# Kernel tuning notes

Measured on AMD Instinct MI355X. Metric: run time of the kernel, lower is better.

## Reference

```python
import jax, jax.numpy as jnp
import numpy as np

VOCAB = 100000; D = 300; F_NUM = 768
M = 64; N = 16
SURF_L = 4; CTX_L = 50; DOC_L = 100; BODY_L = 200
HEADS = 5


def _conv_relu_avg(x, W, b):
    # x: [B, L, D] tokens-embedded; conv1d (valid) + relu + global avgpool -> [B, F]
    y = jax.lax.conv_general_dilated(x.transpose(0, 2, 1), W, (1,), 'VALID',
                                     dimension_numbers=('NCH', 'OIH', 'NCH'))
    return jax.nn.relu(y + b[None, :, None]).mean(axis=2)


def _mha(q, k, v, num_heads=HEADS):
    # split-head scaled dot-product attention (no learned projections), q:[Lq,D] k,v:[Lk,D]
    Lq, Dm = q.shape
    hd = Dm // num_heads
    qh = q.reshape(Lq, num_heads, hd).transpose(1, 0, 2)
    kh = k.reshape(k.shape[0], num_heads, hd).transpose(1, 0, 2)
    vh = v.reshape(v.shape[0], num_heads, hd).transpose(1, 0, 2)
    att = jax.nn.softmax(jnp.einsum('hqd,hkd->hqk', qh, kh) * (1.0 / np.sqrt(hd)), axis=-1)
    out = jnp.einsum('hqk,hkd->hqd', att, vh)
    return out.transpose(1, 0, 2).reshape(Lq, Dm)


def _cos(a, b, eps=1e-6):
    na = jnp.maximum(jnp.sqrt((a * a).sum(-1)), eps)
    nb = jnp.maximum(jnp.sqrt((b * b).sum(-1)), eps)
    return (a * b).sum(-1) / (na * nb)


def setup_inputs() -> dict:
    key = jax.random.key(0)
    ks = jax.random.split(key, 20)
    inp = {}
    inp['mention_entity'] = jnp.ones((M, N), dtype=jnp.int32)
    inp['m'] = M
    inp['n'] = N
    inp['mention_vec'] = jax.random.randint(ks[0], (M, SURF_L), 0, VOCAB)
    inp['context_vec'] = jax.random.randint(ks[1], (M, CTX_L), 0, VOCAB)
    inp['doc_vec'] = jax.random.randint(ks[2], (DOC_L,), 0, VOCAB)
    inp['title_vec'] = jax.random.normal(ks[3], (N, F_NUM), dtype=jnp.float32)
    inp['body_vec'] = jax.random.randint(ks[4], (N, BODY_L), 0, VOCAB)
    inp['sfeats'] = jnp.zeros((N, 1), dtype=jnp.float32)
    inp['m2c_prior'] = jax.random.uniform(ks[5], (N,), dtype=jnp.float32)
    inp['men2cands'] = jax.random.randint(ks[6], (M, N), 0, VOCAB)
    inp['contexts_ids'] = jax.random.randint(ks[7], (M, CTX_L), 0, VOCAB)
    inp['hand_features'] = jax.random.uniform(ks[8], (N, 1), dtype=jnp.float32)
    inp['bert_doc_vec'] = jax.random.normal(ks[9], (1, F_NUM), dtype=jnp.float32)
    # learned parameters
    inp['embed_table'] = jax.random.normal(ks[10], (VOCAB, D), dtype=jnp.float32) * 0.1
    inp['conv_ms_w'] = jax.random.normal(ks[11], (F_NUM, D, 2), dtype=jnp.float32) * 0.05
    inp['conv_ms_b'] = jnp.zeros((F_NUM,), dtype=jnp.float32)
    inp['conv_mc_w'] = jax.random.normal(ks[12], (F_NUM, D, 5), dtype=jnp.float32) * 0.05
    inp['conv_mc_b'] = jnp.zeros((F_NUM,), dtype=jnp.float32)
    inp['layer_local_w'] = jax.random.normal(ks[13], (7,), dtype=jnp.float32) * 0.3
    inp['layer_local_b'] = jnp.zeros((), dtype=jnp.float32)
    inp['att_w1'] = jax.random.normal(ks[14], (600, 300), dtype=jnp.float32) * 0.05
    inp['att_b1'] = jnp.zeros((300,), dtype=jnp.float32)
    inp['att_w2'] = jax.random.normal(ks[15], (300, 1), dtype=jnp.float32) * 0.05
    inp['att_b2'] = jnp.zeros((), dtype=jnp.float32)
    return inp


def reference(mention_entity, m, n, mention_vec, context_vec, doc_vec, title_vec,
              body_vec, sfeats, m2c_prior, men2cands, contexts_ids, hand_features,
              bert_doc_vec, embed_table, conv_ms_w, conv_ms_b, conv_mc_w, conv_mc_b,
              layer_local_w, layer_local_b, att_w1, att_b1, att_w2, att_b2):
    # per-mention conv features (vectorized over all mentions at once)
    ms = _conv_relu_avg(embed_table[mention_vec], conv_ms_w, conv_ms_b)   # [M,768]
    mc = _conv_relu_avg(embed_table[context_vec], conv_mc_w, conv_mc_b)   # [M,768]
    md = bert_doc_vec[0]                                                  # [768]
    doc_emb = embed_table[doc_vec]                                        # [100,300]
    body_emb = embed_table[body_vec]                                      # [N,200,300]

    # per-candidate cross attention doc<->body, max-pooled over query positions
    att_d_b = jax.vmap(lambda b: _mha(doc_emb, b, b).max(axis=0))(body_emb)          # [N,300]
    att_b_d = jax.vmap(lambda b: _mha(b, doc_emb, doc_emb).max(axis=0))(body_emb)    # [N,300]
    comb = jnp.concatenate([att_d_b, att_b_d], axis=-1)                              # [N,600]
    att_score = jax.nn.sigmoid(jax.nn.relu(comb @ att_w1 + att_b1) @ att_w2 + att_b2)[:, 0]  # [N]

    # LocalCtxAttRanker: candidate-vs-context attention score
    ctx_emb = embed_table[contexts_ids]                                   # [M,50,300]
    cand_emb = embed_table[men2cands]                                     # [M,N,300]
    tok = jnp.einsum('mnd,mtd->mnt', cand_emb, ctx_emb)                   # [M,N,50]
    p = jax.nn.softmax(tok.max(axis=1), axis=-1)                          # [M,50]
    ctxv = jnp.einsum('mt,mtd->md', p, ctx_emb)                           # [M,300]
    local_att = jnp.einsum('mnd,md->mn', cand_emb, ctxv)                  # [M,N]

    cos_st = _cos(ms[:, None, :], title_vec[None, :, :])                  # [M,N]
    cos_dt = _cos(md[None, :], title_vec)                                 # [N]
    cos_ct = _cos(mc[:, None, :], title_vec[None, :, :])                  # [M,N]

    Mm = ms.shape[0]
    bc = lambda v: jnp.broadcast_to(v[None, :], (Mm, v.shape[0]))
    # feature order matches torch.cat((hand_fea, prior, localAtt, attScore, C_score))
    feats = jnp.stack([bc(hand_features[:, 0]), bc(m2c_prior), local_att,
                       bc(att_score), cos_st, bc(cos_dt), cos_ct], axis=-1)  # [M,N,7]
    score = feats @ layer_local_w + layer_local_b                         # [M,N]

    # per-mention standardization (unbiased std, as torch.std), softmax and uniform renorm
    mu = score.mean(axis=1, keepdims=True)
    sd = score.std(axis=1, keepdims=True, ddof=1)
    z = (score - mu) / sd
    sm = jax.nn.softmax(z, axis=1)
    zmin = z.min(axis=1, keepdims=True)
    zmax = z.max(axis=1, keepdims=True)
    u = (z + 1.0 - zmin) / (zmax - zmin)
    u = u / u.sum(axis=1, keepdims=True)
    return (z, sm, u)
```

## Files before the change

kernel.cpp:

```cpp
#include <hip/hip_runtime.h>

#define MM 64
#define NN 16
#define DDIM 300
#define FNUM 768
#define SURF_LL 4
#define CTX_LL 50
#define DOC_LL 100
#define BODY_LL 200
#define NHEADS 5
#define HDIM 60

#define GM 2944
#define GK 1536
#define GN 768

typedef unsigned short u16;
typedef unsigned int u32;
typedef __attribute__((ext_vector_type(8))) short short8;
typedef __attribute__((ext_vector_type(4))) float f32x4;

#define OFF_MSG    0
#define OFF_CTX2G  76800
#define OFF_CANDG  1036800
#define OFF_MS     1344000
#define OFF_MC     1393152
#define OFF_PV0    1442304
#define OFF_PV1    1451904
#define OFF_ASC    1471104
#define OFF_LATT   1471120
#define OFF_ABF    1472144
#define OFF_WTMC   (OFF_ABF + GM*GK/2)
#define OFF_WTMS   (OFF_WTMC + GN*GK/2)
#define OFF_P      (OFF_WTMS + 600*768)

__device__ __forceinline__ u16 f2bf(float x) {
  union { float f; u32 u; } v; v.f = x;
  u32 r = v.u + 0x7FFFu + ((v.u >> 16) & 1u);
  return (u16)(r >> 16);
}

__global__ __launch_bounds__(256) void mega_prep_kernel(
    const float* __restrict__ embed,
    const int* __restrict__ mention_vec,
    const int* __restrict__ context_vec,
    const int* __restrict__ contexts_ids,
    const int* __restrict__ men2cands,
    const float* __restrict__ Wmc,
    const float* __restrict__ Wms,
    float* __restrict__ dst, float* __restrict__ mc,
    u32* __restrict__ Abf, u32* __restrict__ WTmc, float* __restrict__ WTms) {
  int bid = blockIdx.x;
  if (bid < 5250) {
    int e = bid * 256 + threadIdx.x;
    int row = e / DDIM;
    int col = e - row * DDIM;
    int tok;
    if (row < 256)       tok = mention_vec[row];
    else if (row < 3456) tok = contexts_ids[row - 256];
    else                 tok = men2cands[row - 3456];
    dst[e] = embed[(size_t)tok * DDIM + col];
  } else if (bid < 5442) {
    mc[(bid - 5250) * 256 + threadIdx.x] = 0.f;
  } else if (bid < 14274) {
    int idx = (bid - 5442) * 256 + threadIdx.x;
    int r = idx / (GK / 2);
    int kp = idx - r * (GK / 2);
    int k = kp * 2;
    int m = r / 46, t = r - m * 46;
    u32 out = 0;
#pragma unroll
    for (int j = 0; j < 2; j++) {
      int kj = k + j;
      u16 h = 0;
      if (kj < 1500) {
        int tap = kj / 300;
        int d = kj - tap * 300;
        int tok = context_vec[m * CTX_LL + t + tap];
        h = f2bf(embed[(size_t)tok * DDIM + d]);
      }
      out |= (u32)h << (16 * j);
    }
    Abf[idx] = out;
  } else if (bid < 16578) {
    int idx = (bid - 14274) * 256 + threadIdx.x;
    int n = idx / (GK / 2);
    int kp = idx - n * (GK / 2);
    int k = kp * 2;
    u32 out = 0;
#pragma unroll
    for (int j = 0; j < 2; j++) {
      int kj = k + j;
      u16 h = 0;
      if (kj < 1500) {
        int tap = kj / 300;
        int d = kj - tap * 300;
        h = f2bf(Wmc[(size_t)n * 1500 + d * 5 + tap]);
      }
      out |= (u32)h << (16 * j);
    }
    WTmc[idx] = out;
  } else {
    int idx = (bid - 16578) * 256 + threadIdx.x;
    int k = idx / FNUM;
    int f = idx - k * FNUM;
    WTms[idx] = Wms[(size_t)f * 600 + k];
  }
}

__global__ __launch_bounds__(256) void conv_gemm_kernel(
    const u16* __restrict__ A,
    const u16* __restrict__ B,
    const float* __restrict__ bias,
    float* __restrict__ mc) {
  int bn = blockIdx.x, bm = blockIdx.y;
  __shared__ u16 As[64][72];
  __shared__ u16 Bs[64][72];
  int tid = threadIdx.x;
  int w = tid >> 6, lane = tid & 63;
  int wr = w >> 1, wc = w & 1;
  int lg = lane >> 4, lm = lane & 15;
  f32x4 acc[2][2];
#pragma unroll
  for (int i = 0; i < 2; i++)
#pragma unroll
    for (int j = 0; j < 2; j++) acc[i][j] = (f32x4)0.f;
  int c0row = tid >> 3, ck = (tid & 7) * 8;
  const u16* Ag = A + (size_t)(bm * 64) * GK;
  const u16* Bg = B + (size_t)(bn * 64) * GK;
  for (int kt = 0; kt < GK / 64; kt++) {
    int k0 = kt * 64;
    uint4 av0 = *(const uint4*)(Ag + (size_t)c0row * GK + k0 + ck);
    uint4 av1 = *(const uint4*)(Ag + (size_t)(c0row + 32) * GK + k0 + ck);
    uint4 bv0 = *(const uint4*)(Bg + (size_t)c0row * GK + k0 + ck);
    uint4 bv1 = *(const uint4*)(Bg + (size_t)(c0row + 32) * GK + k0 + ck);
    __syncthreads();
    *(uint4*)&As[c0row][ck] = av0;
    *(uint4*)&As[c0row + 32][ck] = av1;
    *(uint4*)&Bs[c0row][ck] = bv0;
    *(uint4*)&Bs[c0row + 32][ck] = bv1;
    __syncthreads();
#pragma unroll
    for (int kk = 0; kk < 2; kk++) {
      short8 af0 = *(const short8*)&As[wr * 32 + lm][kk * 32 + lg * 8];
      short8 af1 = *(const short8*)&As[wr * 32 + 16 + lm][kk * 32 + lg * 8];
      short8 bf0 = *(const short8*)&Bs[wc * 32 + lm][kk * 32 + lg * 8];
      short8 bf1 = *(const short8*)&Bs[wc * 32 + 16 + lm][kk * 32 + lg * 8];
      acc[0][0] = __builtin_amdgcn_mfma_f32_16x16x32_bf16(af0, bf0, acc[0][0], 0, 0, 0);
      acc[0][1] = __builtin_amdgcn_mfma_f32_16x16x32_bf16(af0, bf1, acc[0][1], 0, 0, 0);
      acc[1][0] = __builtin_amdgcn_mfma_f32_16x16x32_bf16(af1, bf0, acc[1][0], 0, 0, 0);
      acc[1][1] = __builtin_amdgcn_mfma_f32_16x16x32_bf16(af1, bf1, acc[1][1], 0, 0, 0);
    }
  }
#pragma unroll
  for (int mf = 0; mf < 2; mf++)
#pragma unroll
    for (int nf = 0; nf < 2; nf++) {
      int col = bn * 64 + wc * 32 + nf * 16 + lm;
      float bb = bias[col];
      int base = bm * 64 + wr * 32 + mf * 16 + lg * 4;
      int mcur = base / 46;
      float s = 0.f;
#pragma unroll
      for (int r = 0; r < 4; r++) {
        float v = fmaxf(acc[mf][nf][r] + bb, 0.f) * (1.0f / 46.0f);
        int mm = (base + r) / 46;
        if (mm != mcur) { atomicAdd(&mc[mcur * FNUM + col], s); s = 0.f; mcur = mm; }
        s += v;
      }
      atomicAdd(&mc[mcur * FNUM + col], s);
    }
}

__device__ __forceinline__ void conv_ms_body(
    const float* __restrict__ msg, const float* __restrict__ WT,
    const float* __restrict__ B, float* __restrict__ ms, int b) {
  int m = b / 3, fi = b - m * 3;
  int f = fi * 256 + threadIdx.x;
  const float* x = msg + m * SURF_LL * DDIM;
  float a0 = 0.f, a1 = 0.f, a2 = 0.f;
  for (int d = 0; d < DDIM; d++) {
    float v0 = x[d], v1 = x[DDIM + d], v2 = x[2 * DDIM + d], v3 = x[3 * DDIM + d];
    float wA = WT[(size_t)(2 * d) * FNUM + f];
    float wB = WT[(size_t)(2 * d + 1) * FNUM + f];
    a0 += v0 * wA + v1 * wB;
    a1 += v1 * wA + v2 * wB;
    a2 += v2 * wA + v3 * wB;
  }
  float bb = B[f];
  float r = fmaxf(a0 + bb, 0.f) + fmaxf(a1 + bb, 0.f) + fmaxf(a2 + bb, 0.f);
  ms[m * FNUM + f] = r * (1.0f / 3.0f);
}

template <int DIR>
__device__ __forceinline__ void scores_body(
    const float* __restrict__ embed, const int* __restrict__ doc_vec,
    const int* __restrict__ body_vec, float* __restrict__ P, int b,
    float* __restrict__ smem) {
  constexpr int Lq = DIR ? 200 : 100;
  constexpr int Lk = DIR ? 100 : 200;
  constexpr int KPL = DIR ? 2 : 4;
  int qt = b / 80;
  int rem = b - qt * 80;
  int n = rem / 5, h = rem - n * 5;
  const int* qids = DIR ? body_vec + n * BODY_LL : doc_vec;
  const int* kids = DIR ? doc_vec : body_vec + n * BODY_LL;
  float* Ks = smem;
  float* Qs = smem + Lk * 62;
  for (int idx = threadIdx.x; idx < Lk * 15; idx += 256) {
    int r = idx / 15, c = idx - r * 15;
    float4 v = *(const float4*)(embed + (size_t)kids[r] * DDIM + h * HDIM + c * 4);
    float* dp = Ks + r * 62 + c * 4;
    dp[0] = v.x; dp[1] = v.y; dp[2] = v.z; dp[3] = v.w;
  }
  for (int idx = threadIdx.x; idx < 32 * 15; idx += 256) {
    int r = idx / 15, c = idx - r * 15;
    int q = qt * 32 + r; if (q >= Lq) q = Lq - 1;
    float4 v = *(const float4*)(embed + (size_t)qids[q] * DDIM + h * HDIM + c * 4);
    float* dp = Qs + r * 64 + c * 4;
    dp[0] = v.x; dp[1] = v.y; dp[2] = v.z; dp[3] = v.w;
  }
  __syncthreads();
  int w = threadIdx.x >> 6, lane = threadIdx.x & 63;
  int kcl[KPL];
#pragma unroll
  for (int j = 0; j < KPL; j++) {
    int kk = lane + 64 * j; kcl[j] = (kk < Lk) ? kk : (Lk - 1);
  }
  float acc[8][KPL];
#pragma unroll
  for (int i = 0; i < 8; i++)
#pragma unroll
    for (int j = 0; j < KPL; j++) acc[i][j] = 0.f;
  for (int d = 0; d < HDIM; d += 4) {
    float2 kva[KPL], kvb[KPL];
#pragma unroll
    for (int j = 0; j < KPL; j++) {
      kva[j] = *(const float2*)&Ks[kcl[j] * 62 + d];
      kvb[j] = *(const float2*)&Ks[kcl[j] * 62 + d + 2];
    }
#pragma unroll
    for (int i = 0; i < 8; i++) {
      float4 qv = *(const float4*)&Qs[(w * 8 + i) * 64 + d];
#pragma unroll
      for (int j = 0; j < KPL; j++)
        acc[i][j] += qv.x * kva[j].x + qv.y * kva[j].y +
                     qv.z * kvb[j].x + qv.w * kvb[j].y;
    }
  }
  const float scale = 0.12909944487358056f;
#pragma unroll
  for (int i = 0; i < 8; i++) {
    int q = qt * 32 + w * 8 + i;
    float mx = -1e30f;
#pragma unroll
    for (int j = 0; j < KPL; j++)
      if (lane + 64 * j < Lk) mx = fmaxf(mx, acc[i][j]);
#pragma unroll
    for (int o = 32; o >= 1; o >>= 1) mx = fmaxf(mx, __shfl_xor(mx, o));
    float mxs = mx * scale;
    float p[KPL];
    float s = 0.f;
#pragma unroll
    for (int j = 0; j < KPL; j++) {
      p[j] = (lane + 64 * j < Lk) ? __expf(acc[i][j] * scale - mxs) : 0.f;
      s += p[j];
    }
#pragma unroll
    for (int o = 32; o >= 1; o >>= 1) s += __shfl_xor(s, o);
    float inv = 1.0f / s;
    if (q < Lq) {
      float* rowp = P + (size_t)((n * 2 + DIR) * NHEADS + h) * 20000 + q * Lk;
#pragma unroll
      for (int j = 0; j < KPL; j++) {
        int kk = lane + 64 * j;
        if (kk < Lk) rowp[kk] = p[j] * inv;
      }
    }
  }
}

__device__ __forceinline__ void tokctxv_body(
    const float* __restrict__ candg, const float* __restrict__ ctx2g,
    float* __restrict__ local_att, int m, float* __restrict__ smem) {
  float* cand  = smem;
  float* ctx   = smem + 4800;
  float* tokb  = smem + 9600;
  float* tkmx  = smem + 9872;
  float* pp    = smem + 9936;
  float* sctxv = smem + 10000;
  int tid = threadIdx.x;
  for (int i = tid; i < NN * DDIM; i += 256)
    cand[i] = candg[(size_t)m * NN * DDIM + i];
  int nI = tid >> 4, tt = tid & 15;
  for (int tile = 0; tile < 4; tile++) {
    int cbase = tile * 16;
    __syncthreads();
    for (int i = tid; i < 16 * DDIM; i += 256) {
      int rr = i / DDIM, cc = i - rr * DDIM;
      int t = cbase + rr;
      ctx[rr * DDIM + cc] = (t < CTX_LL) ? ctx2g[(size_t)(m * CTX_LL + t) * DDIM + cc] : 0.f;
    }
    __syncthreads();
    const float4* ca = (const float4*)(cand + nI * DDIM);
    const float4* cb = (const float4*)(ctx + tt * DDIM);
    float dsum = 0.f;
#pragma unroll
    for (int c = 0; c < 75; c++) {
      float4 a = ca[c], b = cb[c];
      dsum += a.x * b.x + a.y * b.y + a.z * b.z + a.w * b.w;
    }
    tokb[nI * 17 + tt] = dsum;
    __syncthreads();
    if (tid < 16) {
      float mx = -1e30f;
      for (int nn = 0; nn < NN; nn++) mx = fmaxf(mx, tokb[nn * 17 + tid]);
      int t = cbase + tid;
      if (t < CTX_LL) tkmx[t] = mx;
    }
  }
  __syncthreads();
  if (tid < 64) {
    float v = (tid < CTX_LL) ? tkmx[tid] : -1e30f;
    float mx = v;
#pragma unroll
    for (int o = 32; o >= 1; o >>= 1) mx = fmaxf(mx, __shfl_xor(mx, o));
    float e = (tid < CTX_LL) ? expf(v - mx) : 0.f;
    float s = e;
#pragma unroll
    for (int o = 32; o >= 1; o >>= 1) s += __shfl_xor(s, o);
    pp[tid] = e / s;
  }
  __syncthreads();
  for (int d = tid; d < DDIM; d += 256) {
    float acc = 0.f;
    for (int t = 0; t < CTX_LL; t++)
      acc += pp[t] * ctx2g[(size_t)(m * CTX_LL + t) * DDIM + d];
    sctxv[d] = acc;
  }
  __syncthreads();
  int j = tid & 15;
  float dd = 0.f;
  for (int i = j; i < DDIM; i += 16) dd += cand[nI * DDIM + i] * sctxv[i];
#pragma unroll
  for (int o = 8; o >= 1; o >>= 1) dd += __shfl_xor(dd, o);
  if (j == 0) local_att[m * NN + nI] = dd;
}

__global__ __launch_bounds__(256) void mega_mid_kernel(
    const float* __restrict__ embed,
    const int* __restrict__ doc_vec,
    const int* __restrict__ body_vec,
    const float* __restrict__ msg,
    const float* __restrict__ WTms,
    const float* __restrict__ Bms,
    const float* __restrict__ candg,
    const float* __restrict__ ctx2g,
    float* __restrict__ ms,
    float* __restrict__ P,
    float* __restrict__ local_att) {
  __shared__ float smem[14448];
  int bid = blockIdx.x;
  if (bid < 192) {
    conv_ms_body(msg, WTms, Bms, ms, bid);
  } else if (bid < 512) {
    scores_body<0>(embed, doc_vec, body_vec, P, bid - 192, smem);
  } else if (bid < 1072) {
    scores_body<1>(embed, doc_vec, body_vec, P, bid - 512, smem);
  } else {
    tokctxv_body(candg, ctx2g, local_att, bid - 1072, smem);
  }
}

__global__ __launch_bounds__(256) void attn_pv_kernel(
    const float* __restrict__ embed,
    const int* __restrict__ doc_vec,
    const int* __restrict__ body_vec,
    const float* __restrict__ P,
    float* __restrict__ pv0,
    float* __restrict__ pv1) {
  int bid = blockIdx.x;
  int dir, pt, n, h;
  if (bid < 160) { dir = 0; h = bid % 5; n = (bid / 5) % 16; pt = bid / 80; }
  else { int b = bid - 160; dir = 1; h = b % 5; n = (b / 5) % 16; pt = b / 80; }
  int Lq = dir ? 200 : 100;
  int Lk = dir ? 100 : 200;
  int Lk4 = Lk >> 2;
  int K4STR = dir ? 27 : 51;
  const int* kids = dir ? doc_vec : body_vec + n * BODY_LL;
  __shared__ float4 Kt4[60 * 51];
  __shared__ float red[4][64];
  float* Ktf = (float*)Kt4;
  int RS = K4STR * 4;
  for (int idx = threadIdx.x; idx < Lk * 15; idx += 256) {
    int r = idx / 15, c = idx - r * 15;
    float4 v = *(const float4*)(embed + (size_t)kids[r] * DDIM + h * HDIM + c * 4);
    Ktf[(c * 4 + 0) * RS + r] = v.x;
    Ktf[(c * 4 + 1) * RS + r] = v.y;
    Ktf[(c * 4 + 2) * RS + r] = v.z;
    Ktf[(c * 4 + 3) * RS + r] = v.w;
  }
  __syncthreads();
  int lane = threadIdx.x & 63;
  int w = __builtin_amdgcn_readfirstlane(threadIdx.x >> 6);
  int dl = (lane < HDIM) ? lane : (HDIM - 1);
  const float4* Krow = Kt4 + dl * K4STR;
  const float* Pb = P + (size_t)((n * 2 + dir) * NHEADS + h) * 20000;
  float omax = -1e30f;
#pragma unroll
  for (int p = 0; p < 4; p++) {
    int q0 = pt * 64 + p * 16 + w * 4;
    int qa0 = min(q0, Lq - 1), qa1 = min(q0 + 1, Lq - 1);
    int qa2 = min(q0 + 2, Lq - 1), qa3 = min(q0 + 3, Lq - 1);
    const float4* P0 = (const float4*)(Pb + (size_t)qa0 * Lk);
    const float4* P1 = (const float4*)(Pb + (size_t)qa1 * Lk);
    const float4* P2 = (const float4*)(Pb + (size_t)qa2 * Lk);
    const float4* P3 = (const float4*)(Pb + (size_t)qa3 * Lk);
    float o0 = 0.f, o1 = 0.f, o2 = 0.f, o3 = 0.f;
    for (int k4 = 0; k4 < Lk4; k4++) {
      float4 pp0 = P0[k4], pp1 = P1[k4], pp2 = P2[k4], pp3 = P3[k4];
      float4 kk = Krow[k4];
      o0 += pp0.x * kk.x + pp0.y * kk.y + pp0.z * kk.z + pp0.w * kk.w;
      o1 += pp1.x * kk.x + pp1.y * kk.y + pp1.z * kk.z + pp1.w * kk.w;
      o2 += pp2.x * kk.x + pp2.y * kk.y + pp2.z * kk.z + pp2.w * kk.w;
      o3 += pp3.x * kk.x + pp3.y * kk.y + pp3.z * kk.z + pp3.w * kk.w;
    }
    if (q0 < Lq)     omax = fmaxf(omax, o0);
    if (q0 + 1 < Lq) omax = fmaxf(omax, o1);
    if (q0 + 2 < Lq) omax = fmaxf(omax, o2);
    if (q0 + 3 < Lq) omax = fmaxf(omax, o3);
  }
  red[threadIdx.x >> 6][lane] = omax;
  __syncthreads();
  if (threadIdx.x < 64 && lane < HDIM) {
    float m4 = fmaxf(fmaxf(red[0][lane], red[1][lane]),
                     fmaxf(red[2][lane], red[3][lane]));
    float* dst = dir ? pv1 + (size_t)((n * NHEADS + h) * 4 + pt) * HDIM
                     : pv0 + (size_t)((n * NHEADS + h) * 2 + pt) * HDIM;
    dst[lane] = m4;
  }
}

__global__ __launch_bounds__(256) void mlp_kernel(
    const float* __restrict__ pv0, const float* __restrict__ pv1,
    const float* __restrict__ w1, const float* __restrict__ b1,
    const float* __restrict__ w2, const float* __restrict__ b2,
    float* __restrict__ att_score) {
  int n = blockIdx.x, tid = threadIdx.x;
  __shared__ float comb[600];
  for (int idx = tid; idx < 300; idx += 256) {
    int h = idx / 60, d = idx - h * 60;
    float mx = -1e30f;
#pragma unroll
    for (int pt = 0; pt < 2; pt++)
      mx = fmaxf(mx, pv0[(size_t)((n * NHEADS + h) * 2 + pt) * HDIM + d]);
    comb[idx] = mx;
    mx = -1e30f;
#pragma unroll
    for (int pt = 0; pt < 4; pt++)
      mx = fmaxf(mx, pv1[(size_t)((n * NHEADS + h) * 4 + pt) * HDIM + d]);
    comb[300 + idx] = mx;
  }
  __syncthreads();
  float partial = 0.f;
  for (int j = tid; j < 300; j += 256) {
    float hh = b1[j];
    for (int k = 0; k < 600; k++) hh += comb[k] * w1[k * 300 + j];
    partial += fmaxf(hh, 0.f) * w2[j];
  }
  __shared__ float redd[256];
  redd[tid] = partial;
  __syncthreads();
  for (int s = 128; s > 0; s >>= 1) {
    if (tid < s) redd[tid] += redd[tid + s];
    __syncthreads();
  }
  if (tid == 0) att_score[n] = 1.0f / (1.0f + expf(-(redd[0] + b2[0])));
}

__global__ __launch_bounds__(256) void final_kernel(
    const float* __restrict__ ms,
    const float* __restrict__ mc,
    const float* __restrict__ title,
    const float* __restrict__ bert,
    const float* __restrict__ att_score,
    const float* __restrict__ m2c_prior,
    const float* __restrict__ hand,
    const float* __restrict__ local_att,
    const float* __restrict__ w7,
    const float* __restrict__ b7,
    float* __restrict__ out) {
  int m = blockIdx.x, tid = threadIdx.x;
  __shared__ float sms[FNUM], smc[FNUM], smd[FNUM];
  __shared__ float snorm[3], sscore[16], wred[3][4];
  for (int i = tid; i < FNUM; i += 256) {
    sms[i] = ms[m * FNUM + i];
    smc[i] = mc[m * FNUM + i];
    smd[i] = bert[i];
  }
  __syncthreads();
  float p1 = 0.f, p2 = 0.f, p3 = 0.f;
  for (int i = tid; i < FNUM; i += 256) {
    float a = sms[i], b = smc[i], c = smd[i];
    p1 += a * a; p2 += b * b; p3 += c * c;
  }
#pragma unroll
  for (int o = 32; o >= 1; o >>= 1) {
    p1 += __shfl_xor(p1, o); p2 += __shfl_xor(p2, o); p3 += __shfl_xor(p3, o);
  }
  int wid = tid >> 6, lane = tid & 63;
  if (lane == 0) { wred[0][wid] = p1; wred[1][wid] = p2; wred[2][wid] = p3; }
  __syncthreads();
  if (tid == 0) {
    snorm[0] = fmaxf(sqrtf(wred[0][0] + wred[0][1] + wred[0][2] + wred[0][3]), 1e-6f);
    snorm[1] = fmaxf(sqrtf(wred[1][0] + wred[1][1] + wred[1][2] + wred[1][3]), 1e-6f);
    snorm[2] = fmaxf(sqrtf(wred[2][0] + wred[2][1] + wred[2][2] + wred[2][3]), 1e-6f);
  }
  __syncthreads();
  int nI = tid >> 4, j = tid & 15;
  float d1 = 0.f, d2 = 0.f, d3 = 0.f, d4 = 0.f;
  for (int i = j; i < FNUM; i += 16) {
    float t = title[nI * FNUM + i];
    d1 += sms[i] * t; d2 += smc[i] * t; d3 += smd[i] * t; d4 += t * t;
  }
#pragma unroll
  for (int o = 8; o >= 1; o >>= 1) {
    d1 += __shfl_xor(d1, o); d2 += __shfl_xor(d2, o);
    d3 += __shfl_xor(d3, o); d4 += __shfl_xor(d4, o);
  }
  if (j == 0) {
    float nt = fmaxf(sqrtf(d4), 1e-6f);
    float cos_st = d1 / (snorm[0] * nt);
    float cos_ct = d2 / (snorm[1] * nt);
    float cos_dt = d3 / (snorm[2] * nt);
    float score = hand[nI] * w7[0] + m2c_prior[nI] * w7[1] +
                  local_att[m * NN + nI] * w7[2] + att_score[nI] * w7[3] +
                  cos_st * w7[4] + cos_dt * w7[5] + cos_ct * w7[6] + b7[0];
    sscore[nI] = score;
  }
  __syncthreads();
  if (tid < 16) {
    float x = sscore[tid];
    float s = x;
#pragma unroll
    for (int o = 8; o >= 1; o >>= 1) s += __shfl_xor(s, o);
    float mu = s * (1.0f / 16.0f);
    float dv = (x - mu) * (x - mu);
    float vs = dv;
#pragma unroll
    for (int o = 8; o >= 1; o >>= 1) vs += __shfl_xor(vs, o);
    float sd = sqrtf(vs * (1.0f / 15.0f));
    float z = (x - mu) / sd;
    float zm = z;
#pragma unroll
    for (int o = 8; o >= 1; o >>= 1) zm = fmaxf(zm, __shfl_xor(zm, o));
    float e = expf(z - zm);
    float es = e;
#pragma unroll
    for (int o = 8; o >= 1; o >>= 1) es += __shfl_xor(es, o);
    float sm = e / es;
    float zmin = z;
#pragma unroll
    for (int o = 8; o >= 1; o >>= 1) zmin = fminf(zmin, __shfl_xor(zmin, o));
    float u0 = (z + 1.0f - zmin) / (zm - zmin);
    float us = u0;
#pragma unroll
    for (int o = 8; o >= 1; o >>= 1) us += __shfl_xor(us, o);
    float u = u0 / us;
    out[m * NN + tid] = z;
    out[MM * NN + m * NN + tid] = sm;
    out[2 * MM * NN + m * NN + tid] = u;
  }
}

extern "C" void kernel_launch(void* const* d_in, const int* in_sizes, int n_in,
                              void* d_out, int out_size, void* d_ws, size_t ws_size,
                              hipStream_t stream) {
  const int*   mention_vec   = (const int*)d_in[3];
  const int*   context_vec   = (const int*)d_in[4];
  const int*   doc_vec       = (const int*)d_in[5];
  const float* title_vec     = (const float*)d_in[6];
  const int*   body_vec      = (const int*)d_in[7];
  const float* m2c_prior     = (const float*)d_in[9];
  const int*   men2cands     = (const int*)d_in[10];
  const int*   contexts_ids  = (const int*)d_in[11];
  const float* hand_features = (const float*)d_in[12];
  const float* bert_doc_vec  = (const float*)d_in[13];
  const float* embed_table   = (const float*)d_in[14];
  const float* conv_ms_w     = (const float*)d_in[15];
  const float* conv_ms_b     = (const float*)d_in[16];
  const float* conv_mc_w     = (const float*)d_in[17];
  const float* conv_mc_b     = (const float*)d_in[18];
  const float* layer_local_w = (const float*)d_in[19];
  const float* layer_local_b = (const float*)d_in[20];
  const float* att_w1        = (const float*)d_in[21];
  const float* att_b1        = (const float*)d_in[22];
  const float* att_w2        = (const float*)d_in[23];
  const float* att_b2        = (const float*)d_in[24];

  float* ws     = (float*)d_ws;
  float* msg    = ws + OFF_MSG;
  float* ctx2g  = ws + OFF_CTX2G;
  float* candg  = ws + OFF_CANDG;
  float* ms     = ws + OFF_MS;
  float* mc     = ws + OFF_MC;
  float* pv0    = ws + OFF_PV0;
  float* pv1    = ws + OFF_PV1;
  float* att_sc = ws + OFF_ASC;
  float* latt   = ws + OFF_LATT;
  u16*   Abf    = (u16*)(ws + OFF_ABF);
  u16*   WTmc   = (u16*)(ws + OFF_WTMC);
  float* WTms   = ws + OFF_WTMS;
  float* P      = ws + OFF_P;
  float* out    = (float*)d_out;

  mega_prep_kernel<<<dim3(18378), dim3(256), 0, stream>>>(
      embed_table, mention_vec, context_vec, contexts_ids, men2cands,
      conv_mc_w, conv_ms_w, ws, mc, (u32*)Abf, (u32*)WTmc, WTms);
  conv_gemm_kernel<<<dim3(GN / 64, GM / 64), dim3(256), 0, stream>>>(
      Abf, WTmc, conv_mc_b, mc);
  mega_mid_kernel<<<dim3(1136), dim3(256), 0, stream>>>(
      embed_table, doc_vec, body_vec, msg, WTms, conv_ms_b, candg, ctx2g,
      ms, P, latt);
  attn_pv_kernel<<<dim3(480), dim3(256), 0, stream>>>(
      embed_table, doc_vec, body_vec, P, pv0, pv1);
  mlp_kernel<<<dim3(NN), dim3(256), 0, stream>>>(pv0, pv1, att_w1, att_b1, att_w2, att_b2, att_sc);
  final_kernel<<<dim3(MM), dim3(256), 0, stream>>>(
      ms, mc, title_vec, bert_doc_vec, att_sc, m2c_prior, hand_features,
      latt, layer_local_w, layer_local_b, out);
}
```

Baseline: 417.6 us.

## Shrink mid-kernel shared memory via chunked transposed K tiles and reorder blocks

```diff
diff --git a/kernel.cpp b/kernel.cpp
--- a/kernel.cpp
+++ b/kernel.cpp
@@ -199,72 +199,69 @@
     float* __restrict__ smem) {
   constexpr int Lq = DIR ? 200 : 100;
   constexpr int Lk = DIR ? 100 : 200;
-  constexpr int KPL = DIR ? 2 : 4;
+  constexpr int NPASS = DIR ? 1 : 2;
   int qt = b / 80;
   int rem = b - qt * 80;
   int n = rem / 5, h = rem - n * 5;
   const int* qids = DIR ? body_vec + n * BODY_LL : doc_vec;
   const int* kids = DIR ? doc_vec : body_vec + n * BODY_LL;
-  float* Ks = smem;
-  float* Qs = smem + Lk * 62;
-  for (int idx = threadIdx.x; idx < Lk * 15; idx += 256) {
-    int r = idx / 15, c = idx - r * 15;
-    float4 v = *(const float4*)(embed + (size_t)kids[r] * DDIM + h * HDIM + c * 4);
-    float* dp = Ks + r * 62 + c * 4;
-    dp[0] = v.x; dp[1] = v.y; dp[2] = v.z; dp[3] = v.w;
-  }
+  float4* Kt4 = (float4*)smem;
+  float* Qs = smem + 6000;
   for (int idx = threadIdx.x; idx < 32 * 15; idx += 256) {
     int r = idx / 15, c = idx - r * 15;
     int q = qt * 32 + r; if (q >= Lq) q = Lq - 1;
     float4 v = *(const float4*)(embed + (size_t)qids[q] * DDIM + h * HDIM + c * 4);
-    float* dp = Qs + r * 64 + c * 4;
-    dp[0] = v.x; dp[1] = v.y; dp[2] = v.z; dp[3] = v.w;
-  }
-  __syncthreads();
+    *(float4*)&Qs[r * 64 + c * 4] = v;
+  }
   int w = threadIdx.x >> 6, lane = threadIdx.x & 63;
-  int kcl[KPL];
-#pragma unroll
-  for (int j = 0; j < KPL; j++) {
-    int kk = lane + 64 * j; kcl[j] = (kk < Lk) ? kk : (Lk - 1);
-  }
-  float acc[8][KPL];
+  int k1 = (lane < 36) ? (64 + lane) : 99;
+  float acc[8][2 * NPASS];
 #pragma unroll
   for (int i = 0; i < 8; i++)
 #pragma unroll
-    for (int j = 0; j < KPL; j++) acc[i][j] = 0.f;
-  for (int d = 0; d < HDIM; d += 4) {
-    float2 kva[KPL], kvb[KPL];
-#pragma unroll
-    for (int j = 0; j < KPL; j++) {
-      kva[j] = *(const float2*)&Ks[kcl[j] * 62 + d];
-      kvb[j] = *(const float2*)&Ks[kcl[j] * 62 + d + 2];
-    }
-#pragma unroll
-    for (int i = 0; i < 8; i++) {
-      float4 qv = *(const float4*)&Qs[(w * 8 + i) * 64 + d];
-#pragma unroll
-      for (int j = 0; j < KPL; j++)
-        acc[i][j] += qv.x * kva[j].x + qv.y * kva[j].y +
-                     qv.z * kvb[j].x + qv.w * kvb[j].y;
+    for (int j = 0; j < 2 * NPASS; j++) acc[i][j] = 0.f;
+#pragma unroll
+  for (int p = 0; p < NPASS; p++) {
+    __syncthreads();
+    for (int idx = threadIdx.x; idx < 1500; idx += 256) {
+      int c = idx / 100, r = idx - c * 100;
+      float4 v = *(const float4*)(embed + (size_t)kids[p * 100 + r] * DDIM + h * HDIM + c * 4);
+      Kt4[c * 100 + r] = v;
+    }
+    __syncthreads();
+#pragma unroll
+    for (int c = 0; c < 15; c++) {
+      float4 k0 = Kt4[c * 100 + lane];
+      float4 kv1 = Kt4[c * 100 + k1];
+#pragma unroll
+      for (int i = 0; i < 8; i++) {
+        float4 qv = *(const float4*)&Qs[(w * 8 + i) * 64 + c * 4];
+        acc[i][p * 2 + 0] += qv.x * k0.x + qv.y * k0.y + qv.z * k0.z + qv.w * k0.w;
+        acc[i][p * 2 + 1] += qv.x * kv1.x + qv.y * kv1.y + qv.z * kv1.z + qv.w * kv1.w;
+      }
     }
   }
   const float scale = 0.12909944487358056f;
+  bool v1 = (lane < 36);
 #pragma unroll
   for (int i = 0; i < 8; i++) {
     int q = qt * 32 + w * 8 + i;
     float mx = -1e30f;
 #pragma unroll
-    for (int j = 0; j < KPL; j++)
-      if (lane + 64 * j < Lk) mx = fmaxf(mx, acc[i][j]);
+    for (int p = 0; p < NPASS; p++) {
+      mx = fmaxf(mx, acc[i][p * 2]);
+      if (v1) mx = fmaxf(mx, acc[i][p * 2 + 1]);
+    }
 #pragma unroll
     for (int o = 32; o >= 1; o >>= 1) mx = fmaxf(mx, __shfl_xor(mx, o));
     float mxs = mx * scale;
-    float p[KPL];
+    float pe[2 * NPASS];
     float s = 0.f;
 #pragma unroll
-    for (int j = 0; j < KPL; j++) {
-      p[j] = (lane + 64 * j < Lk) ? __expf(acc[i][j] * scale - mxs) : 0.f;
-      s += p[j];
+    for (int p = 0; p < NPASS; p++) {
+      pe[p * 2] = __expf(acc[i][p * 2] * scale - mxs);
+      pe[p * 2 + 1] = v1 ? __expf(acc[i][p * 2 + 1] * scale - mxs) : 0.f;
+      s += pe[p * 2] + pe[p * 2 + 1];
     }
 #pragma unroll
     for (int o = 32; o >= 1; o >>= 1) s += __shfl_xor(s, o);
@@ -272,9 +269,9 @@
     if (q < Lq) {
       float* rowp = P + (size_t)((n * 2 + DIR) * NHEADS + h) * 20000 + q * Lk;
 #pragma unroll
-      for (int j = 0; j < KPL; j++) {
-        int kk = lane + 64 * j;
-        if (kk < Lk) rowp[kk] = p[j] * inv;
+      for (int p = 0; p < NPASS; p++) {
+        rowp[p * 100 + lane] = pe[p * 2] * inv;
+        if (v1) rowp[p * 100 + 64 + lane] = pe[p * 2 + 1] * inv;
       }
     }
   }
@@ -283,16 +280,14 @@
 __device__ __forceinline__ void tokctxv_body(
     const float* __restrict__ candg, const float* __restrict__ ctx2g,
     float* __restrict__ local_att, int m, float* __restrict__ smem) {
-  float* cand  = smem;
-  float* ctx   = smem + 4800;
-  float* tokb  = smem + 9600;
-  float* tkmx  = smem + 9872;
-  float* pp    = smem + 9936;
-  float* sctxv = smem + 10000;
+  float* ctx   = smem;
+  float* tokb  = smem + 4800;
+  float* tkmx  = smem + 5072;
+  float* pp    = smem + 5136;
+  float* sctxv = smem + 5200;
   int tid = threadIdx.x;
-  for (int i = tid; i < NN * DDIM; i += 256)
-    cand[i] = candg[(size_t)m * NN * DDIM + i];
   int nI = tid >> 4, tt = tid & 15;
+  const float4* ca = (const float4*)(candg + (size_t)(m * NN + nI) * DDIM);
   for (int tile = 0; tile < 4; tile++) {
     int cbase = tile * 16;
     __syncthreads();
@@ -302,7 +297,6 @@
       ctx[rr * DDIM + cc] = (t < CTX_LL) ? ctx2g[(size_t)(m * CTX_LL + t) * DDIM + cc] : 0.f;
     }
     __syncthreads();
-    const float4* ca = (const float4*)(cand + nI * DDIM);
     const float4* cb = (const float4*)(ctx + tt * DDIM);
     float dsum = 0.f;
 #pragma unroll
@@ -340,8 +334,9 @@
   }
   __syncthreads();
   int j = tid & 15;
+  const float* crow = candg + (size_t)(m * NN + nI) * DDIM;
   float dd = 0.f;
-  for (int i = j; i < DDIM; i += 16) dd += cand[nI * DDIM + i] * sctxv[i];
+  for (int i = j; i < DDIM; i += 16) dd += crow[i] * sctxv[i];
 #pragma unroll
   for (int o = 8; o >= 1; o >>= 1) dd += __shfl_xor(dd, o);
   if (j == 0) local_att[m * NN + nI] = dd;
@@ -359,16 +354,16 @@
     float* __restrict__ ms,
     float* __restrict__ P,
     float* __restrict__ local_att) {
-  __shared__ float smem[14448];
+  __shared__ float smem[8048];
   int bid = blockIdx.x;
-  if (bid < 192) {
-    conv_ms_body(msg, WTms, Bms, ms, bid);
-  } else if (bid < 512) {
-    scores_body<0>(embed, doc_vec, body_vec, P, bid - 192, smem);
-  } else if (bid < 1072) {
-    scores_body<1>(embed, doc_vec, body_vec, P, bid - 512, smem);
+  if (bid < 64) {
+    tokctxv_body(candg, ctx2g, local_att, bid, smem);
+  } else if (bid < 384) {
+    scores_body<0>(embed, doc_vec, body_vec, P, bid - 64, smem);
+  } else if (bid < 944) {
+    scores_body<1>(embed, doc_vec, body_vec, P, bid - 384, smem);
   } else {
-    tokctxv_body(candg, ctx2g, local_att, bid - 1072, smem);
+    conv_ms_body(msg, WTms, Bms, ms, bid - 944);
   }
 }
 
```

After: 514.0 us. +23.1%, slower.

## Split DIR0 scores into own kernel and shrink mid-kernel shared memory

Applied to the files above, without the earlier changes.

```diff
diff --git a/kernel.cpp b/kernel.cpp
--- a/kernel.cpp
+++ b/kernel.cpp
@@ -172,6 +172,96 @@
     }
 }
 
+template <int DIR>
+__device__ __forceinline__ void scores_body(
+    const float* __restrict__ embed, const int* __restrict__ doc_vec,
+    const int* __restrict__ body_vec, float* __restrict__ P, int b,
+    float* __restrict__ smem) {
+  constexpr int Lq = DIR ? 200 : 100;
+  constexpr int Lk = DIR ? 100 : 200;
+  constexpr int KPL = DIR ? 2 : 4;
+  int qt = b / 80;
+  int rem = b - qt * 80;
+  int n = rem / 5, h = rem - n * 5;
+  const int* qids = DIR ? body_vec + n * BODY_LL : doc_vec;
+  const int* kids = DIR ? doc_vec : body_vec + n * BODY_LL;
+  float* Ks = smem;
+  float* Qs = smem + Lk * 61;
+  for (int idx = threadIdx.x; idx < Lk * 15; idx += 256) {
+    int r = idx / 15, c = idx - r * 15;
+    float4 v = *(const float4*)(embed + (size_t)kids[r] * DDIM + h * HDIM + c * 4);
+    float* dp = Ks + r * 61 + c * 4;
+    dp[0] = v.x; dp[1] = v.y; dp[2] = v.z; dp[3] = v.w;
+  }
+  for (int idx = threadIdx.x; idx < 32 * 15; idx += 256) {
+    int r = idx / 15, c = idx - r * 15;
+    int q = qt * 32 + r; if (q >= Lq) q = Lq - 1;
+    float4 v = *(const float4*)(embed + (size_t)qids[q] * DDIM + h * HDIM + c * 4);
+    float* dp = Qs + r * 61 + c * 4;
+    dp[0] = v.x; dp[1] = v.y; dp[2] = v.z; dp[3] = v.w;
+  }
+  __syncthreads();
+  int w = threadIdx.x >> 6, lane = threadIdx.x & 63;
+  float acc[8][KPL];
+#pragma unroll
+  for (int i = 0; i < 8; i++)
+#pragma unroll
+    for (int j = 0; j < KPL; j++) acc[i][j] = 0.f;
+  for (int d = 0; d < HDIM; d++) {
+    float kv[KPL];
+#pragma unroll
+    for (int j = 0; j < KPL; j++) {
+      int kk = lane + 64 * j; if (kk >= Lk) kk = Lk - 1;
+      kv[j] = Ks[kk * 61 + d];
+    }
+#pragma unroll
+    for (int i = 0; i < 8; i++) {
+      float qv = Qs[(w * 8 + i) * 61 + d];
+#pragma unroll
+      for (int j = 0; j < KPL; j++) acc[i][j] += qv * kv[j];
+    }
+  }
+  const float scale = 0.12909944487358056f;
+#pragma unroll
+  for (int i = 0; i < 8; i++) {
+    int q = qt * 32 + w * 8 + i;
+    float mx = -1e30f;
+#pragma unroll
+    for (int j = 0; j < KPL; j++)
+      if (lane + 64 * j < Lk) mx = fmaxf(mx, acc[i][j]);
+#pragma unroll
+    for (int o = 32; o >= 1; o >>= 1) mx = fmaxf(mx, __shfl_xor(mx, o));
+    float mxs = mx * scale;
+    float p[KPL];
+    float s = 0.f;
+#pragma unroll
+    for (int j = 0; j < KPL; j++) {
+      p[j] = (lane + 64 * j < Lk) ? __expf(acc[i][j] * scale - mxs) : 0.f;
+      s += p[j];
+    }
+#pragma unroll
+    for (int o = 32; o >= 1; o >>= 1) s += __shfl_xor(s, o);
+    float inv = 1.0f / s;
+    if (q < Lq) {
+      float* rowp = P + (size_t)((n * 2 + DIR) * NHEADS + h) * 20000 + q * Lk;
+#pragma unroll
+      for (int j = 0; j < KPL; j++) {
+        int kk = lane + 64 * j;
+        if (kk < Lk) rowp[kk] = p[j] * inv;
+      }
+    }
+  }
+}
+
+__global__ __launch_bounds__(256) void scores0_kernel(
+    const float* __restrict__ embed,
+    const int* __restrict__ doc_vec,
+    const int* __restrict__ body_vec,
+    float* __restrict__ P) {
+  __shared__ float smem[(200 + 32) * 61];
+  scores_body<0>(embed, doc_vec, body_vec, P, blockIdx.x, smem);
+}
+
 __device__ __forceinline__ void conv_ms_body(
     const float* __restrict__ msg, const float* __restrict__ WT,
     const float* __restrict__ B, float* __restrict__ ms, int b) {
@@ -192,107 +282,17 @@
   ms[m * FNUM + f] = r * (1.0f / 3.0f);
 }
 
-template <int DIR>
-__device__ __forceinline__ void scores_body(
-    const float* __restrict__ embed, const int* __restrict__ doc_vec,
-    const int* __restrict__ body_vec, float* __restrict__ P, int b,
-    float* __restrict__ smem) {
-  constexpr int Lq = DIR ? 200 : 100;
-  constexpr int Lk = DIR ? 100 : 200;
-  constexpr int KPL = DIR ? 2 : 4;
-  int qt = b / 80;
-  int rem = b - qt * 80;
-  int n = rem / 5, h = rem - n * 5;
-  const int* qids = DIR ? body_vec + n * BODY_LL : doc_vec;
-  const int* kids = DIR ? doc_vec : body_vec + n * BODY_LL;
-  float* Ks = smem;
-  float* Qs = smem + Lk * 62;
-  for (int idx = threadIdx.x; idx < Lk * 15; idx += 256) {
-    int r = idx / 15, c = idx - r * 15;
-    float4 v = *(const float4*)(embed + (size_t)kids[r] * DDIM + h * HDIM + c * 4);
-    float* dp = Ks + r * 62 + c * 4;
-    dp[0] = v.x; dp[1] = v.y; dp[2] = v.z; dp[3] = v.w;
-  }
-  for (int idx = threadIdx.x; idx < 32 * 15; idx += 256) {
-    int r = idx / 15, c = idx - r * 15;
-    int q = qt * 32 + r; if (q >= Lq) q = Lq - 1;
-    float4 v = *(const float4*)(embed + (size_t)qids[q] * DDIM + h * HDIM + c * 4);
-    float* dp = Qs + r * 64 + c * 4;
-    dp[0] = v.x; dp[1] = v.y; dp[2] = v.z; dp[3] = v.w;
-  }
-  __syncthreads();
-  int w = threadIdx.x >> 6, lane = threadIdx.x & 63;
-  int kcl[KPL];
-#pragma unroll
-  for (int j = 0; j < KPL; j++) {
-    int kk = lane + 64 * j; kcl[j] = (kk < Lk) ? kk : (Lk - 1);
-  }
-  float acc[8][KPL];
-#pragma unroll
-  for (int i = 0; i < 8; i++)
-#pragma unroll
-    for (int j = 0; j < KPL; j++) acc[i][j] = 0.f;
-  for (int d = 0; d < HDIM; d += 4) {
-    float2 kva[KPL], kvb[KPL];
-#pragma unroll
-    for (int j = 0; j < KPL; j++) {
-      kva[j] = *(const float2*)&Ks[kcl[j] * 62 + d];
-      kvb[j] = *(const float2*)&Ks[kcl[j] * 62 + d + 2];
-    }
-#pragma unroll
-    for (int i = 0; i < 8; i++) {
-      float4 qv = *(const float4*)&Qs[(w * 8 + i) * 64 + d];
-#pragma unroll
-      for (int j = 0; j < KPL; j++)
-        acc[i][j] += qv.x * kva[j].x + qv.y * kva[j].y +
-                     qv.z * kvb[j].x + qv.w * kvb[j].y;
-    }
-  }
-  const float scale = 0.12909944487358056f;
-#pragma unroll
-  for (int i = 0; i < 8; i++) {
-    int q = qt * 32 + w * 8 + i;
-    float mx = -1e30f;
-#pragma unroll
-    for (int j = 0; j < KPL; j++)
-      if (lane + 64 * j < Lk) mx = fmaxf(mx, acc[i][j]);
-#pragma unroll
-    for (int o = 32; o >= 1; o >>= 1) mx = fmaxf(mx, __shfl_xor(mx, o));
-    float mxs = mx * scale;
-    float p[KPL];
-    float s = 0.f;
-#pragma unroll
-    for (int j = 0; j < KPL; j++) {
-      p[j] = (lane + 64 * j < Lk) ? __expf(acc[i][j] * scale - mxs) : 0.f;
-      s += p[j];
-    }
-#pragma unroll
-    for (int o = 32; o >= 1; o >>= 1) s += __shfl_xor(s, o);
-    float inv = 1.0f / s;
-    if (q < Lq) {
-      float* rowp = P + (size_t)((n * 2 + DIR) * NHEADS + h) * 20000 + q * Lk;
-#pragma unroll
-      for (int j = 0; j < KPL; j++) {
-        int kk = lane + 64 * j;
-        if (kk < Lk) rowp[kk] = p[j] * inv;
-      }
-    }
-  }
-}
-
 __device__ __forceinline__ void tokctxv_body(
     const float* __restrict__ candg, const float* __restrict__ ctx2g,
     float* __restrict__ local_att, int m, float* __restrict__ smem) {
-  float* cand  = smem;
-  float* ctx   = smem + 4800;
-  float* tokb  = smem + 9600;
-  float* tkmx  = smem + 9872;
-  float* pp    = smem + 9936;
-  float* sctxv = smem + 10000;
+  float* ctx   = smem;
+  float* tokb  = smem + 4800;
+  float* tkmx  = smem + 5072;
+  float* pp    = smem + 5136;
+  float* sctxv = smem + 5200;
   int tid = threadIdx.x;
-  for (int i = tid; i < NN * DDIM; i += 256)
-    cand[i] = candg[(size_t)m * NN * DDIM + i];
   int nI = tid >> 4, tt = tid & 15;
+  const float4* ca = (const float4*)(candg + (size_t)(m * NN + nI) * DDIM);
   for (int tile = 0; tile < 4; tile++) {
     int cbase = tile * 16;
     __syncthreads();
@@ -302,7 +302,6 @@
       ctx[rr * DDIM + cc] = (t < CTX_LL) ? ctx2g[(size_t)(m * CTX_LL + t) * DDIM + cc] : 0.f;
     }
     __syncthreads();
-    const float4* ca = (const float4*)(cand + nI * DDIM);
     const float4* cb = (const float4*)(ctx + tt * DDIM);
     float dsum = 0.f;
 #pragma unroll
@@ -340,8 +339,9 @@
   }
   __syncthreads();
   int j = tid & 15;
+  const float* crow = candg + (size_t)(m * NN + nI) * DDIM;
   float dd = 0.f;
-  for (int i = j; i < DDIM; i += 16) dd += cand[nI * DDIM + i] * sctxv[i];
+  for (int i = j; i < DDIM; i += 16) dd += crow[i] * sctxv[i];
 #pragma unroll
   for (int o = 8; o >= 1; o >>= 1) dd += __shfl_xor(dd, o);
   if (j == 0) local_att[m * NN + nI] = dd;
@@ -359,16 +359,14 @@
     float* __restrict__ ms,
     float* __restrict__ P,
     float* __restrict__ local_att) {
-  __shared__ float smem[14448];
+  __shared__ float smem[(100 + 32) * 61];
   int bid = blockIdx.x;
-  if (bid < 192) {
-    conv_ms_body(msg, WTms, Bms, ms, bid);
-  } else if (bid < 512) {
-    scores_body<0>(embed, doc_vec, body_vec, P, bid - 192, smem);
-  } else if (bid < 1072) {
-    scores_body<1>(embed, doc_vec, body_vec, P, bid - 512, smem);
+  if (bid < 64) {
+    tokctxv_body(candg, ctx2g, local_att, bid, smem);
+  } else if (bid < 624) {
+    scores_body<1>(embed, doc_vec, body_vec, P, bid - 64, smem);
   } else {
-    tokctxv_body(candg, ctx2g, local_att, bid - 1072, smem);
+    conv_ms_body(msg, WTms, Bms, ms, bid - 624);
   }
 }
 
@@ -619,7 +617,9 @@
       conv_mc_w, conv_ms_w, ws, mc, (u32*)Abf, (u32*)WTmc, WTms);
   conv_gemm_kernel<<<dim3(GN / 64, GM / 64), dim3(256), 0, stream>>>(
       Abf, WTmc, conv_mc_b, mc);
-  mega_mid_kernel<<<dim3(1136), dim3(256), 0, stream>>>(
+  scores0_kernel<<<dim3(320), dim3(256), 0, stream>>>(
+      embed_table, doc_vec, body_vec, P);
+  mega_mid_kernel<<<dim3(816), dim3(256), 0, stream>>>(
       embed_table, doc_vec, body_vec, msg, WTms, conv_ms_b, candg, ctx2g,
       ms, P, latt);
   attn_pv_kernel<<<dim3(480), dim3(256), 0, stream>>>(
```

Result: slower. 437.0 us (+4.6%).
